# Performance work log

Hardware: AMD Instinct MI355X
Metric: run time of the kernel (lower is better)

Reference implementation:

```python
import jax, jax.numpy as jnp
import numpy as np

H, DK, D, DFF = 8, 64, 512, 512
B, S = 4, 1024
SCALE = 1.0 / np.sqrt(DK)


def _ln(x, g, b, eps=1e-5):
    m = jnp.mean(x, axis=-1, keepdims=True)
    v = jnp.mean((x - m) ** 2, axis=-1, keepdims=True)
    return (x - m) / jnp.sqrt(v + eps) * g + b


def _heads(x, w, b):
    bs, s, _ = x.shape
    return (x @ w + b).reshape(bs, s, H, DK).transpose(0, 2, 1, 3)  # [B,H,S,DK]


def _encoder_layer(x, qw, qb, kw, kb, vw, vb, ow, ob, g1, b1, w1, c1, w2, c2, g2, b2):
    # standard post-LN transformer encoder layer (sub_attention.Encoder(1))
    q = _heads(x, qw, qb)
    k = _heads(x, kw, kb)
    v = _heads(x, vw, vb)
    attn = jax.nn.softmax(jnp.einsum('bhqd,bhkd->bhqk', q, k) * SCALE, axis=-1)
    ctx = jnp.einsum('bhqk,bhkd->bhqd', attn, v).transpose(0, 2, 1, 3).reshape(x.shape[0], -1, H * DK)
    h = _ln(ctx @ ow + ob + x, g1, b1)
    f = jax.nn.relu(h @ w1 + c1) @ w2 + c2
    return _ln(f + h, g2, b2)


def setup_inputs() -> dict:
    key = jax.random.key(0)
    ks = iter(jax.random.split(key, 80))

    def nrm(*shape):
        return jax.random.normal(next(ks), shape, jnp.float32) * 0.02

    inp = {'audio_feat': jax.random.normal(next(ks), (B, S, D), jnp.float32),
           'video_feat': jax.random.normal(next(ks), (B, S, D), jnp.float32)}
    for p in ['aq', 'ak', 'av', 'vq', 'vk', 'vv', 'out']:
        inp[p + '_w'] = nrm(D, D)
        inp[p + '_b'] = jnp.zeros((D,), jnp.float32)
    inp['ln_g'] = jnp.ones((D,), jnp.float32)
    inp['ln_b'] = jnp.zeros((D,), jnp.float32)
    for pfx in ['asa_', 'vsa_']:
        for wn in ['qw', 'kw', 'vw', 'ow']:
            inp[pfx + wn] = nrm(D, D)
        for bn in ['qb', 'kb', 'vb', 'ob']:
            inp[pfx + bn] = jnp.zeros((D,), jnp.float32)
        inp[pfx + 'w1'] = nrm(D, DFF)
        inp[pfx + 'c1'] = jnp.zeros((DFF,), jnp.float32)
        inp[pfx + 'w2'] = nrm(DFF, D)
        inp[pfx + 'c2'] = jnp.zeros((D,), jnp.float32)
        inp[pfx + 'g1'] = jnp.ones((D,), jnp.float32)
        inp[pfx + 'b1'] = jnp.zeros((D,), jnp.float32)
        inp[pfx + 'g2'] = jnp.ones((D,), jnp.float32)
        inp[pfx + 'b2'] = jnp.zeros((D,), jnp.float32)
    return inp


def reference(audio_feat, video_feat, aq_w, aq_b, ak_w, ak_b, av_w, av_b, vq_w, vq_b, vk_w, vk_b, vv_w, vv_b, out_w, out_b, ln_g, ln_b, asa_qw, asa_qb, asa_kw, asa_kb, asa_vw, asa_vb, asa_ow, asa_ob, asa_g1, asa_b1, asa_w1, asa_c1, asa_w2, asa_c2, asa_g2, asa_b2, vsa_qw, vsa_qb, vsa_kw, vsa_kb, vsa_vw, vsa_vb, vsa_ow, vsa_ob, vsa_g1, vsa_b1, vsa_w1, vsa_c1, vsa_w2, vsa_c2, vsa_g2, vsa_b2):
    audio_self = _encoder_layer(audio_feat, asa_qw, asa_qb, asa_kw, asa_kb, asa_vw, asa_vb, asa_ow, asa_ob, asa_g1, asa_b1, asa_w1, asa_c1, asa_w2, asa_c2, asa_g2, asa_b2)
    video_self = _encoder_layer(video_feat, vsa_qw, vsa_qb, vsa_kw, vsa_kb, vsa_vw, vsa_vb, vsa_ow, vsa_ob, vsa_g1, vsa_b1, vsa_w1, vsa_c1, vsa_w2, vsa_c2, vsa_g2, vsa_b2)
    qa = _heads(audio_feat, aq_w, aq_b)
    ka = _heads(audio_feat, ak_w, ak_b)
    va = _heads(audio_feat, av_w, av_b)
    qv = _heads(video_feat, vq_w, vq_b)
    kv = _heads(video_feat, vk_w, vk_b)
    vvh = _heads(video_feat, vv_w, vv_b)
    attn_a = jax.nn.softmax(jnp.einsum('bhqd,bhkd->bhqk', qa, ka) * SCALE, axis=-1)
    attn_v = jax.nn.softmax(jnp.einsum('bhqd,bhkd->bhqk', qv, kv) * SCALE, axis=-1)
    attn = attn_a * attn_v  # dual-softmax elementwise combine
    ctx = jnp.einsum('bhqk,bhkd->bhqd', attn, va) * jnp.einsum('bhqk,bhkd->bhqd', attn, vvh)
    ctx = ctx.transpose(0, 2, 1, 3).reshape(audio_feat.shape[0], -1, H * DK)
    context = ctx @ out_w + out_b
    return _ln(audio_feat + context + audio_self + video_self, ln_g, ln_b)
```

## Files before the change

### kernel.cpp

```cpp
#include <hip/hip_runtime.h>
#include <cstddef>
#include <cstdint>


typedef __attribute__((ext_vector_type(8))) short s8v;
typedef __attribute__((ext_vector_type(4))) float f4v;

#define QSC 0.1803368801111444f
#define EXP2(x) __builtin_amdgcn_exp2f(x)
#define WAITV(N) asm volatile("s_waitcnt vmcnt(" #N ")" ::: "memory")
#define BAR() __builtin_amdgcn_s_barrier()

static __device__ __forceinline__ short f2bf(float f){
  unsigned int u = __builtin_bit_cast(unsigned int, f);
  u += 0x7fffu + ((u >> 16) & 1u);
  return (short)(u >> 16);
}
static __device__ __forceinline__ float bf2f(short s){
  unsigned int u = ((unsigned int)(unsigned short)s) << 16;
  return __builtin_bit_cast(float, u);
}
static __device__ __forceinline__ void gload16(const void* g, void* l){
  __builtin_amdgcn_global_load_lds(
      (const __attribute__((address_space(1))) unsigned int*)g,
      (__attribute__((address_space(3))) unsigned int*)l, 16, 0, 0);
}
#define MFMA16(a,b,c) __builtin_amdgcn_mfma_f32_16x16x32_bf16(a,b,c,0,0,0)

__global__ __launch_bounds__(256) void convert_in(const float* __restrict__ a,
                                                  const float* __restrict__ v,
                                                  short* __restrict__ oa,
                                                  short* __restrict__ ov){
  const float* src = blockIdx.y ? v : a;
  short* dst = blockIdx.y ? ov : oa;
  const int i = (blockIdx.x * 256 + threadIdx.x) * 8;
  float4 x = *reinterpret_cast<const float4*>(src + i);
  float4 y = *reinterpret_cast<const float4*>(src + i + 4);
  s8v o;
  o[0]=f2bf(x.x); o[1]=f2bf(x.y); o[2]=f2bf(x.z); o[3]=f2bf(x.w);
  o[4]=f2bf(y.x); o[5]=f2bf(y.y); o[6]=f2bf(y.z); o[7]=f2bf(y.w);
  *reinterpret_cast<s8v*>(dst + i) = o;
}

struct Ptr19 { const float* p[19]; };
__global__ __launch_bounds__(256) void pack_w(Ptr19 ws, short* __restrict__ wp){
  const int mat = blockIdx.y;
  const float* W = ws.p[mat];
  const int f = blockIdx.x * 256 + threadIdx.x;
  const int nblk = f >> 10, kg = (f >> 4) & 63, nl = f & 15;
  const int n = nblk * 16 + nl, k = kg * 8;
  s8v o;
#pragma unroll
  for (int e = 0; e < 8; ++e) o[e] = f2bf(W[(size_t)(k + e) * 512 + n]);
  *reinterpret_cast<s8v*>(wp + (size_t)mat * 262144 + (size_t)f * 8) = o;
}

struct GemmJobs { const short* A[12]; const short* W[12]; const float* bias[12];
                  short* C[12]; int mode[12]; };

template<bool RELU>
__global__ __launch_bounds__(256) void gemm_bf16(GemmJobs J){
  int i = (blockIdx.z * 32 + blockIdx.y) * 4 + blockIdx.x;
  const int c = (128 * gridDim.z) >> 3;
  i = (i & 7) * c + (i >> 3);
  const int z = i >> 7, rem = i & 127;
  const int by = rem >> 2, bx = rem & 3;

  const short* __restrict__ A = J.A[z];
  const short* __restrict__ Wp = J.W[z];
  const float* __restrict__ bias = J.bias[z];
  short* __restrict__ C = J.C[z];
  const int md = J.mode[z];
  __shared__ short As[2][4096], Bs[2][4096];
  const int tid = threadIdx.x, lane = tid & 63, w = tid >> 6;
  const int wm = w >> 1, wn = w & 1;
  const int m0 = by * 128, n0 = bx * 128;
  const int lh = lane >> 4, ll = lane & 15;
  f4v acc[4][4] = {};

  auto stage = [&](int kt, int buf){
    const int k0 = kt * 32;
#pragma unroll
    for (int p = 0; p < 2; ++p){
      const int f = tid + 256 * p;
      const int blk = f >> 6, kg = (f >> 4) & 3, il = f & 15;
      gload16(A + (size_t)(m0 + blk * 16 + il) * 512 + k0 + kg * 8, &As[buf][f * 8]);
      gload16(Wp + ((size_t)(((n0 >> 4) + blk) * 64 + (k0 >> 3) + kg) * 16 + il) * 8,
              &Bs[buf][f * 8]);
    }
  };

  stage(0, 0);
#pragma unroll
  for (int kt = 0; kt < 16; ++kt){
    if (kt < 15) { stage(kt + 1, (kt + 1) & 1); WAITV(4); }
    else         { WAITV(0); }
    BAR();
    const int cur = kt & 1;
    s8v a[4], b[4];
#pragma unroll
    for (int q = 0; q < 4; ++q)
      a[q] = *reinterpret_cast<const s8v*>(&As[cur][(((wm*4+q)*4 + lh)*16 + ll) * 8]);
#pragma unroll
    for (int j = 0; j < 4; ++j)
      b[j] = *reinterpret_cast<const s8v*>(&Bs[cur][(((wn*4+j)*4 + lh)*16 + ll) * 8]);
#pragma unroll
    for (int q = 0; q < 4; ++q)
#pragma unroll
      for (int j = 0; j < 4; ++j)
        acc[q][j] = MFMA16(a[q], b[j], acc[q][j]);
    BAR();
  }

  if (md == 2){
#pragma unroll
    for (int j = 0; j < 4; ++j){
      const int col = n0 + wn * 64 + j * 16 + ll;
      const float bv = bias[col];
      const int hh = col >> 6, dl = col & 63, dblk = dl >> 4, il = dl & 15;
#pragma unroll
      for (int q = 0; q < 4; ++q){
        const int rowb = m0 + wm * 64 + q * 16 + lh * 4;
#pragma unroll
        for (int r = 0; r < 4; ++r){
          const int m = rowb + r;
          const int bb = m >> 10, srow = m & 1023;
          const size_t off = ((size_t)((bb*8 + hh)*16 + (srow >> 6))) * 4096
                           + (size_t)(((dblk << 7) + (((srow >> 3) & 7) << 4) + il) * 8 + (srow & 7));
          C[off] = f2bf(acc[q][j][r] + bv);
        }
      }
    }
  } else {
    const float sc = (md == 1) ? QSC : 1.0f;
#pragma unroll
    for (int j = 0; j < 4; ++j){
      const int col = n0 + wn * 64 + j * 16 + ll;
      const float bv = bias[col];
#pragma unroll
      for (int q = 0; q < 4; ++q){
        const int rowb = m0 + wm * 64 + q * 16 + lh * 4;
#pragma unroll
        for (int r = 0; r < 4; ++r){
          float v = (acc[q][j][r] + bv) * sc;
          if (RELU) v = fmaxf(v, 0.f);
          C[(size_t)(rowb + r) * 512 + col] = f2bf(v);
        }
      }
    }
  }
}

template<bool RELU>
__global__ __launch_bounds__(256) void gemm_n64(GemmJobs J){
  int i = (blockIdx.z * 32 + blockIdx.y) * 8 + blockIdx.x;
  const int c = (256 * gridDim.z) >> 3;
  i = (i & 7) * c + (i >> 3);
  const int z = i >> 8, rem = i & 255;
  const int by = rem >> 3, bx = rem & 7;

  const short* __restrict__ A = J.A[z];
  const short* __restrict__ Wp = J.W[z];
  const float* __restrict__ bias = J.bias[z];
  short* __restrict__ C = J.C[z];
  __shared__ short As[2][4096], Bs[2][2048];
  const int tid = threadIdx.x, lane = tid & 63, w = tid >> 6;
  const int wm = w >> 1, wn = w & 1;
  const int m0 = by * 128, n0 = bx * 64;
  const int lh = lane >> 4, ll = lane & 15;
  f4v acc[4][2] = {};

  auto stage = [&](int kt, int buf){
    const int k0 = kt * 32;
#pragma unroll
    for (int p = 0; p < 2; ++p){
      const int f = tid + 256 * p;
      const int blk = f >> 6, kg = (f >> 4) & 3, il = f & 15;
      gload16(A + (size_t)(m0 + blk * 16 + il) * 512 + k0 + kg * 8, &As[buf][f * 8]);
    }
    {
      const int f = tid;
      const int blk = f >> 6, kg = (f >> 4) & 3, il = f & 15;
      gload16(Wp + ((size_t)(((n0 >> 4) + blk) * 64 + (k0 >> 3) + kg) * 16 + il) * 8,
              &Bs[buf][f * 8]);
    }
  };

  stage(0, 0);
#pragma unroll
  for (int kt = 0; kt < 16; ++kt){
    if (kt < 15) { stage(kt + 1, (kt + 1) & 1); WAITV(3); }
    else         { WAITV(0); }
    BAR();
    const int cur = kt & 1;
    s8v a[4], b[2];
#pragma unroll
    for (int q = 0; q < 4; ++q)
      a[q] = *reinterpret_cast<const s8v*>(&As[cur][(((wm*4+q)*4 + lh)*16 + ll) * 8]);
#pragma unroll
    for (int j = 0; j < 2; ++j)
      b[j] = *reinterpret_cast<const s8v*>(&Bs[cur][(((wn*2+j)*4 + lh)*16 + ll) * 8]);
#pragma unroll
    for (int q = 0; q < 4; ++q)
#pragma unroll
      for (int j = 0; j < 2; ++j)
        acc[q][j] = MFMA16(a[q], b[j], acc[q][j]);
    BAR();
  }

#pragma unroll
  for (int j = 0; j < 2; ++j){
    const int col = n0 + wn * 32 + j * 16 + ll;
    const float bv = bias[col];
#pragma unroll
    for (int q = 0; q < 4; ++q){
      const int rowb = m0 + wm * 64 + q * 16 + lh * 4;
#pragma unroll
      for (int r = 0; r < 4; ++r){
        float v = acc[q][j][r] + bv;
        if (RELU) v = fmaxf(v, 0.f);
        C[(size_t)(rowb + r) * 512 + col] = f2bf(v);
      }
    }
  }
}

struct AttnJob { const short* Q; const short* K; const short* Vp; short* O; };

__global__ __launch_bounds__(512) void attn_enc(AttnJob j0, AttnJob j1){
  const AttnJob jb = blockIdx.z ? j1 : j0;
  __shared__ short KT[2][4096], VT[2][4096];
  __shared__ short PL[8][1024];
  const int tid = threadIdx.x, lane = tid & 63, w = tid >> 6;
  int bi = blockIdx.y * 8 + blockIdx.x;
  bi = (bi & 7) * 32 + (bi >> 3);
  const int qt = bi & 7, bh = bi >> 3;
  const int b = bh >> 3, h = bh & 7;
  const int q0 = qt * 128;
  const size_t base = (size_t)b * 1024 * 512 + (size_t)h * 64;
  const int lh = lane >> 4, ll = lane & 15;
  short* PLw = PL[w];

  s8v qf[2];
#pragma unroll
  for (int df = 0; df < 2; ++df)
    qf[df] = *reinterpret_cast<const s8v*>(jb.Q + base + (size_t)(q0 + w*16 + ll)*512 + lh*8 + df*32);

  const int sblk = tid >> 7, sg8 = (tid >> 4) & 7, sil = tid & 15;
  auto stage = [&](int it, int buf){
    gload16(jb.K + base + (size_t)(it*64 + sblk*16 + sil)*512 + sg8*8, &KT[buf][tid*8]);
    gload16(jb.Vp + ((size_t)bh*16 + it)*4096 + (size_t)tid*8, &VT[buf][tid*8]);
  };

  f4v o[4] = {};
  float lp[4] = {0.f, 0.f, 0.f, 0.f};

  stage(0, 0);
#pragma unroll 1
  for (int it = 0; it < 16; ++it){
    if (it < 15) { stage(it + 1, (it + 1) & 1); WAITV(2); }
    else         { WAITV(0); }
    BAR();
    const int cur = it & 1;

    f4v s[4] = {};
#pragma unroll
    for (int fn = 0; fn < 4; ++fn)
#pragma unroll
      for (int df = 0; df < 2; ++df){
        s8v kf = *reinterpret_cast<const s8v*>(&KT[cur][((fn*8 + lh + df*4)*16 + ll) * 8]);
        s[fn] = MFMA16(qf[df], kf, s[fn]);
      }

    float px[4][4];
#pragma unroll
    for (int r = 0; r < 4; ++r){
      float p0 = EXP2(s[0][r]), p1 = EXP2(s[1][r]);
      float p2 = EXP2(s[2][r]), p3 = EXP2(s[3][r]);
      px[r][0]=p0; px[r][1]=p1; px[r][2]=p2; px[r][3]=p3;
      lp[r] += (p0 + p1) + (p2 + p3);
    }
#pragma unroll
    for (int r = 0; r < 4; ++r)
#pragma unroll
      for (int fn = 0; fn < 4; ++fn){
        const int q = lh*4 + r, k = fn*16 + ll, kg = k >> 3;
        PLw[(kg*16 + (q ^ kg))*8 + (k & 7)] = f2bf(px[r][fn]);
      }
    s8v pa[2];
#pragma unroll
    for (int kf2 = 0; kf2 < 2; ++kf2){
      const int kg = lh + kf2*4;
      pa[kf2] = *reinterpret_cast<const s8v*>(&PLw[(kg*16 + (ll ^ kg))*8]);
    }
#pragma unroll
    for (int fd = 0; fd < 4; ++fd)
#pragma unroll
      for (int kf2 = 0; kf2 < 2; ++kf2){
        s8v vf = *reinterpret_cast<const s8v*>(&VT[cur][((fd*8 + lh + kf2*4)*16 + ll) * 8]);
        o[fd] = MFMA16(pa[kf2], vf, o[fd]);
      }
    BAR();
  }

#pragma unroll
  for (int r = 0; r < 4; ++r){
    float Z = lp[r];
    Z += __shfl_xor(Z, 1); Z += __shfl_xor(Z, 2);
    Z += __shfl_xor(Z, 4); Z += __shfl_xor(Z, 8);
    const float rz = 1.f / Z;
#pragma unroll
    for (int fd = 0; fd < 4; ++fd)
      jb.O[base + (size_t)(q0 + w*16 + lh*4 + r)*512 + fd*16 + ll] = f2bf(o[fd][r] * rz);
  }
}

__global__ __launch_bounds__(512) void attn_dual(const short* __restrict__ Qa, const short* __restrict__ Ka,
                                                 const short* __restrict__ Vap, const short* __restrict__ Qv,
                                                 const short* __restrict__ Kv, const short* __restrict__ Vvp,
                                                 short* __restrict__ O){
  __shared__ short KTa[2][4096], KTv[2][4096], VTa[2][4096], VTv[2][4096];
  __shared__ short PL[8][1024];
  const int tid = threadIdx.x, lane = tid & 63, w = tid >> 6;
  int bi = blockIdx.y * 8 + blockIdx.x;
  bi = (bi & 7) * 32 + (bi >> 3);
  const int qt = bi & 7, bh = bi >> 3;
  const int b = bh >> 3, h = bh & 7;
  const int q0 = qt * 128;
  const size_t base = (size_t)b * 1024 * 512 + (size_t)h * 64;
  const int lh = lane >> 4, ll = lane & 15;
  short* PLw = PL[w];

  s8v qfa[2], qfv[2];
#pragma unroll
  for (int df = 0; df < 2; ++df){
    const size_t ro = base + (size_t)(q0 + w*16 + ll)*512 + lh*8 + df*32;
    qfa[df] = *reinterpret_cast<const s8v*>(Qa + ro);
    qfv[df] = *reinterpret_cast<const s8v*>(Qv + ro);
  }

  const int sblk = tid >> 7, sg8 = (tid >> 4) & 7, sil = tid & 15;
  auto stage = [&](int it, int buf){
    const size_t krow = base + (size_t)(it*64 + sblk*16 + sil)*512 + sg8*8;
    gload16(Ka + krow, &KTa[buf][tid*8]);
    gload16(Kv + krow, &KTv[buf][tid*8]);
    const size_t voff = ((size_t)bh*16 + it)*4096 + (size_t)tid*8;
    gload16(Vap + voff, &VTa[buf][tid*8]);
    gload16(Vvp + voff, &VTv[buf][tid*8]);
  };

  f4v oa[4] = {}, ov[4] = {};
  float lap[4] = {0,0,0,0}, lvp[4] = {0,0,0,0};

  stage(0, 0);
#pragma unroll 1
  for (int it = 0; it < 16; ++it){
    if (it < 15) { stage(it + 1, (it + 1) & 1); WAITV(4); }
    else         { WAITV(0); }
    BAR();
    const int cur = it & 1;

    f4v sa[4] = {}, sv[4] = {};
#pragma unroll
    for (int fn = 0; fn < 4; ++fn)
#pragma unroll
      for (int df = 0; df < 2; ++df){
        const int boff = ((fn*8 + lh + df*4)*16 + ll) * 8;
        s8v ka = *reinterpret_cast<const s8v*>(&KTa[cur][boff]);
        s8v kv = *reinterpret_cast<const s8v*>(&KTv[cur][boff]);
        sa[fn] = MFMA16(qfa[df], ka, sa[fn]);
        sv[fn] = MFMA16(qfv[df], kv, sv[fn]);
      }

    float pt[4][4];
#pragma unroll
    for (int r = 0; r < 4; ++r){
      float a0 = EXP2(sa[0][r]), a1 = EXP2(sa[1][r]);
      float a2 = EXP2(sa[2][r]), a3 = EXP2(sa[3][r]);
      float v0 = EXP2(sv[0][r]), v1 = EXP2(sv[1][r]);
      float v2 = EXP2(sv[2][r]), v3 = EXP2(sv[3][r]);
      lap[r] += (a0 + a1) + (a2 + a3);
      lvp[r] += (v0 + v1) + (v2 + v3);
      pt[r][0] = a0*v0; pt[r][1] = a1*v1; pt[r][2] = a2*v2; pt[r][3] = a3*v3;
    }
#pragma unroll
    for (int r = 0; r < 4; ++r)
#pragma unroll
      for (int fn = 0; fn < 4; ++fn){
        const int q = lh*4 + r, k = fn*16 + ll, kg = k >> 3;
        PLw[(kg*16 + (q ^ kg))*8 + (k & 7)] = f2bf(pt[r][fn]);
      }
    s8v pa[2];
#pragma unroll
    for (int kf2 = 0; kf2 < 2; ++kf2){
      const int kg = lh + kf2*4;
      pa[kf2] = *reinterpret_cast<const s8v*>(&PLw[(kg*16 + (ll ^ kg))*8]);
    }
#pragma unroll
    for (int fd = 0; fd < 4; ++fd)
#pragma unroll
      for (int kf2 = 0; kf2 < 2; ++kf2){
        const int boff = ((fd*8 + lh + kf2*4)*16 + ll) * 8;
        s8v va = *reinterpret_cast<const s8v*>(&VTa[cur][boff]);
        s8v vv = *reinterpret_cast<const s8v*>(&VTv[cur][boff]);
        oa[fd] = MFMA16(pa[kf2], va, oa[fd]);
        ov[fd] = MFMA16(pa[kf2], vv, ov[fd]);
      }
    BAR();
  }

#pragma unroll
  for (int r = 0; r < 4; ++r){
    float Za = lap[r], Zv = lvp[r];
    Za += __shfl_xor(Za, 1); Za += __shfl_xor(Za, 2);
    Za += __shfl_xor(Za, 4); Za += __shfl_xor(Za, 8);
    Zv += __shfl_xor(Zv, 1); Zv += __shfl_xor(Zv, 2);
    Zv += __shfl_xor(Zv, 4); Zv += __shfl_xor(Zv, 8);
    const float rz = 1.f / (Za * Zv);
#pragma unroll
    for (int fd = 0; fd < 4; ++fd){
      const float v = (oa[fd][r] * rz) * (ov[fd][r] * rz);
      O[base + (size_t)(q0 + w*16 + lh*4 + r)*512 + fd*16 + ll] = f2bf(v);
    }
  }
}

struct LnJob { const short* xb0; const short* xb1; const short* xb2;
               const float* xf; const float* g; const float* bb; void* out; };

template<int NBF, bool ADDF32, bool OUTF32>
__global__ __launch_bounds__(256) void ln_fused(LnJob j0, LnJob j1){
  const LnJob j = blockIdx.y ? j1 : j0;
  const int row = blockIdx.x, t = threadIdx.x;
  const size_t base = (size_t)row * 512;
  float x[2];
#pragma unroll
  for (int u = 0; u < 2; ++u){
    const int c = t + u * 256;
    float v = bf2f(j.xb0[base + c]);
    if (NBF > 1) v += bf2f(j.xb1[base + c]);
    if (NBF > 2) v += bf2f(j.xb2[base + c]);
    if (ADDF32) v += j.xf[base + c];
    x[u] = v;
  }
  float s = x[0] + x[1], ss = x[0]*x[0] + x[1]*x[1];
#pragma unroll
  for (int o = 32; o; o >>= 1){ s += __shfl_xor(s, o); ss += __shfl_xor(ss, o); }
  __shared__ float rb[8];
  const int wv = t >> 6;
  if ((t & 63) == 0){ rb[wv] = s; rb[wv + 4] = ss; }
  __syncthreads();
  s  = rb[0] + rb[1] + rb[2] + rb[3];
  ss = rb[4] + rb[5] + rb[6] + rb[7];
  const float m = s * (1.f / 512.f);
  const float var = ss * (1.f / 512.f) - m * m;
  const float rstd = rsqrtf(var + 1e-5f);
#pragma unroll
  for (int u = 0; u < 2; ++u){
    const int c = t + u * 256;
    const float v = (x[u] - m) * rstd * j.g[c] + j.bb[c];
    if (OUTF32) ((float*)j.out)[base + c] = v;
    else        ((short*)j.out)[base + c] = f2bf(v);
  }
}

extern "C" void kernel_launch(void* const* d_in, const int* in_sizes, int n_in,
                              void* d_out, int out_size, void* d_ws, size_t ws_size,
                              hipStream_t stream) {
  const float* audio = (const float*)d_in[0];
  const float* video = (const float*)d_in[1];
  auto F = [&](int i){ return (const float*)d_in[i]; };

  short* ws16 = (short*)d_ws;
  const size_t SL = 2097152;
  auto S = [&](int i){ return ws16 + (size_t)i * SL; };
  short* Wp = S(12);
  auto WP = [&](int i){ return (const short*)(Wp + (size_t)i * 262144); };
  short* Kcv = (short*)d_out;
  short* Vcv = (short*)d_out + SL;

  convert_in<<<dim3(1024,2), 256, 0, stream>>>(audio, video, S(10), S(11));

  Ptr19 pw;
  const int widx[19] = {18,19,20,21,26,28, 34,35,36,37,42,44, 2,4,6,8,10,12, 14};
  for (int i = 0; i < 19; ++i) pw.p[i] = F(widx[i]);
  pack_w<<<dim3(128,19), 256, 0, stream>>>(pw, Wp);

  GemmJobs g1{};
  const short* g1A[12] = {S(10),S(10),S(10), S(11),S(11),S(11), S(10),S(10),S(10), S(11),S(11),S(11)};
  const short* g1W[12] = {WP(0),WP(1),WP(2), WP(6),WP(7),WP(8), WP(12),WP(13),WP(14), WP(15),WP(16),WP(17)};
  const float* g1B[12] = {F(22),F(23),F(24), F(38),F(39),F(40), F(3),F(5),F(7), F(9),F(11),F(13)};
  short*       g1C[12] = {S(0),S(1),S(2), S(3),S(4),S(5), S(6),S(7),S(8), S(9),Kcv,Vcv};
  const int    g1M[12] = {1,0,2, 1,0,2, 1,0,2, 1,0,2};
  for (int i = 0; i < 12; ++i){ g1.A[i]=g1A[i]; g1.W[i]=g1W[i]; g1.bias[i]=g1B[i]; g1.C[i]=g1C[i]; g1.mode[i]=g1M[i]; }
  gemm_bf16<false><<<dim3(4,32,12), 256, 0, stream>>>(g1);

  attn_enc<<<dim3(8,32,2), 512, 0, stream>>>(AttnJob{S(0),S(1),S(2),S(10)},
                                             AttnJob{S(3),S(4),S(5),S(11)});

  GemmJobs g3{};
  g3.A[0]=S(10); g3.W[0]=WP(3); g3.bias[0]=F(25); g3.C[0]=S(0); g3.mode[0]=0;
  g3.A[1]=S(11); g3.W[1]=WP(9); g3.bias[1]=F(41); g3.C[1]=S(1); g3.mode[1]=0;
  gemm_n64<false><<<dim3(8,32,2), 256, 0, stream>>>(g3);

  ln_fused<1,true,false><<<dim3(4096,2), 256, 0, stream>>>(
      LnJob{S(0),nullptr,nullptr, audio, F(30),F(31), S(2)},
      LnJob{S(1),nullptr,nullptr, video, F(46),F(47), S(3)});

  GemmJobs g5{};
  g5.A[0]=S(2); g5.W[0]=WP(4);  g5.bias[0]=F(27); g5.C[0]=S(4); g5.mode[0]=0;
  g5.A[1]=S(3); g5.W[1]=WP(10); g5.bias[1]=F(43); g5.C[1]=S(5); g5.mode[1]=0;
  gemm_n64<true><<<dim3(8,32,2), 256, 0, stream>>>(g5);

  GemmJobs g6{};
  g6.A[0]=S(4); g6.W[0]=WP(5);  g6.bias[0]=F(29); g6.C[0]=S(0); g6.mode[0]=0;
  g6.A[1]=S(5); g6.W[1]=WP(11); g6.bias[1]=F(45); g6.C[1]=S(1); g6.mode[1]=0;
  gemm_n64<false><<<dim3(8,32,2), 256, 0, stream>>>(g6);

  ln_fused<2,false,false><<<dim3(4096,2), 256, 0, stream>>>(
      LnJob{S(0),S(2),nullptr, nullptr, F(32),F(33), S(4)},
      LnJob{S(1),S(3),nullptr, nullptr, F(48),F(49), S(5)});

  attn_dual<<<dim3(8,32), 512, 0, stream>>>(S(6),S(7),S(8), S(9),Kcv,Vcv, S(3));

  GemmJobs g9{};
  g9.A[0]=S(3); g9.W[0]=WP(18); g9.bias[0]=F(15); g9.C[0]=S(0); g9.mode[0]=0;
  gemm_n64<false><<<dim3(8,32,1), 256, 0, stream>>>(g9);

  LnJob fj{S(0),S(4),S(5), audio, F(16),F(17), d_out};
  ln_fused<3,true,true><<<dim3(4096,1), 256, 0, stream>>>(fj, fj);
}
```

Measured before the change: 200.0 us.

## Stage GEMM epilogues through LDS, merge output GEMMs and fuse final layernorms

The GEMM epilogues now write results into shared memory first and then store them to global memory as 16-byte vectors, replacing scattered 2-byte stores. The head-layout mode writes 4 contiguous shorts per store. The dual-attention kernel moves earlier so its output projection can share one gemm_n64 launch with the two encoder output projections. The second per-encoder layernorm and the final layernorm are folded into one ln_final kernel. Together these cut the launch count and one round trip of intermediate tensors, at the cost of reusing shared buffers and a reshuffled workspace assignment.

```diff
diff --git a/kernel.cpp b/kernel.cpp
--- a/kernel.cpp
+++ b/kernel.cpp
@@ -4,6 +4,7 @@
 
 
 typedef __attribute__((ext_vector_type(8))) short s8v;
+typedef __attribute__((ext_vector_type(4))) short s4v;
 typedef __attribute__((ext_vector_type(4))) float f4v;
 
 #define QSC 0.1803368801111444f
@@ -121,32 +122,35 @@
 #pragma unroll
       for (int q = 0; q < 4; ++q){
         const int rowb = m0 + wm * 64 + q * 16 + lh * 4;
-#pragma unroll
-        for (int r = 0; r < 4; ++r){
-          const int m = rowb + r;
-          const int bb = m >> 10, srow = m & 1023;
-          const size_t off = ((size_t)((bb*8 + hh)*16 + (srow >> 6))) * 4096
-                           + (size_t)(((dblk << 7) + (((srow >> 3) & 7) << 4) + il) * 8 + (srow & 7));
-          C[off] = f2bf(acc[q][j][r] + bv);
-        }
+        const int bb = rowb >> 10, srow = rowb & 1023;
+        const size_t off = ((size_t)((bb*8 + hh)*16 + (srow >> 6))) * 4096
+                         + (size_t)(((dblk << 7) + (((srow >> 3) & 7) << 4) + il) * 8 + (srow & 7));
+        s4v o4;
+#pragma unroll
+        for (int r = 0; r < 4; ++r) o4[r] = f2bf(acc[q][j][r] + bv);
+        *reinterpret_cast<s4v*>(&C[off]) = o4;
       }
     }
   } else {
+    short* epi = (w < 2) ? &As[w][0] : &Bs[w - 2][0];
     const float sc = (md == 1) ? QSC : 1.0f;
 #pragma unroll
     for (int j = 0; j < 4; ++j){
-      const int col = n0 + wn * 64 + j * 16 + ll;
-      const float bv = bias[col];
-#pragma unroll
-      for (int q = 0; q < 4; ++q){
-        const int rowb = m0 + wm * 64 + q * 16 + lh * 4;
+      const float bv = bias[n0 + wn * 64 + j * 16 + ll];
+#pragma unroll
+      for (int q = 0; q < 4; ++q)
 #pragma unroll
         for (int r = 0; r < 4; ++r){
           float v = (acc[q][j][r] + bv) * sc;
           if (RELU) v = fmaxf(v, 0.f);
-          C[(size_t)(rowb + r) * 512 + col] = f2bf(v);
+          epi[(q*16 + lh*4 + r)*64 + j*16 + ll] = f2bf(v);
         }
-      }
+    }
+#pragma unroll
+    for (int i2 = 0; i2 < 8; ++i2){
+      const int row = i2 * 8 + (lane >> 3);
+      s8v vr = *reinterpret_cast<const s8v*>(&epi[row*64 + (lane & 7)*8]);
+      *reinterpret_cast<s8v*>(&C[(size_t)(m0 + wm*64 + row)*512 + n0 + wn*64 + (lane&7)*8]) = vr;
     }
   }
 }
@@ -208,20 +212,24 @@
     BAR();
   }
 
+  short* epi = &As[0][0] + w * 2048;
 #pragma unroll
   for (int j = 0; j < 2; ++j){
-    const int col = n0 + wn * 32 + j * 16 + ll;
-    const float bv = bias[col];
-#pragma unroll
-    for (int q = 0; q < 4; ++q){
-      const int rowb = m0 + wm * 64 + q * 16 + lh * 4;
+    const float bv = bias[n0 + wn * 32 + j * 16 + ll];
+#pragma unroll
+    for (int q = 0; q < 4; ++q)
 #pragma unroll
       for (int r = 0; r < 4; ++r){
         float v = acc[q][j][r] + bv;
         if (RELU) v = fmaxf(v, 0.f);
-        C[(size_t)(rowb + r) * 512 + col] = f2bf(v);
-      }
-    }
+        epi[(q*16 + lh*4 + r)*32 + j*16 + ll] = f2bf(v);
+      }
+  }
+#pragma unroll
+  for (int i2 = 0; i2 < 4; ++i2){
+    const int row = i2 * 16 + (lane >> 2);
+    s8v vr = *reinterpret_cast<const s8v*>(&epi[row*32 + (lane & 3)*8]);
+    *reinterpret_cast<s8v*>(&C[(size_t)(m0 + wm*64 + row)*512 + n0 + wn*32 + (lane&3)*8]) = vr;
   }
 }
 
@@ -464,6 +472,64 @@
   }
 }
 
+__global__ __launch_bounds__(256) void ln_final(const short* __restrict__ fa, const short* __restrict__ ha,
+                                                const short* __restrict__ fv, const short* __restrict__ hv,
+                                                const short* __restrict__ ctx, const float* __restrict__ audio,
+                                                const float* __restrict__ g2a, const float* __restrict__ b2a,
+                                                const float* __restrict__ g2v, const float* __restrict__ b2v,
+                                                const float* __restrict__ gf, const float* __restrict__ bf,
+                                                float* __restrict__ out){
+  const int row = blockIdx.x, t = threadIdx.x;
+  const size_t base = (size_t)row * 512;
+  __shared__ float rb[24];
+  const int wv = t >> 6;
+
+  auto reduce2 = [&](float a, float b, int p){
+    float s = a + b, ss = a*a + b*b;
+#pragma unroll
+    for (int o = 32; o; o >>= 1){ s += __shfl_xor(s, o); ss += __shfl_xor(ss, o); }
+    if ((t & 63) == 0){ rb[p*8 + wv] = s; rb[p*8 + 4 + wv] = ss; }
+  };
+  auto stats = [&](int p, float& m, float& rstd){
+    const float s  = rb[p*8+0] + rb[p*8+1] + rb[p*8+2] + rb[p*8+3];
+    const float ss = rb[p*8+4] + rb[p*8+5] + rb[p*8+6] + rb[p*8+7];
+    m = s * (1.f / 512.f);
+    rstd = rsqrtf(ss * (1.f / 512.f) - m * m + 1e-5f);
+  };
+
+  float xa[2], xv[2];
+#pragma unroll
+  for (int u = 0; u < 2; ++u){
+    const int c = t + u * 256;
+    xa[u] = bf2f(fa[base + c]) + bf2f(ha[base + c]);
+    xv[u] = bf2f(fv[base + c]) + bf2f(hv[base + c]);
+  }
+  reduce2(xa[0], xa[1], 0);
+  reduce2(xv[0], xv[1], 1);
+  __syncthreads();
+  float ma, ra, mv, rv;
+  stats(0, ma, ra);
+  stats(1, mv, rv);
+
+  float xf[2];
+#pragma unroll
+  for (int u = 0; u < 2; ++u){
+    const int c = t + u * 256;
+    const float sa = (xa[u] - ma) * ra * g2a[c] + b2a[c];
+    const float sv = (xv[u] - mv) * rv * g2v[c] + b2v[c];
+    xf[u] = audio[base + c] + bf2f(ctx[base + c]) + sa + sv;
+  }
+  reduce2(xf[0], xf[1], 2);
+  __syncthreads();
+  float mf, rf;
+  stats(2, mf, rf);
+#pragma unroll
+  for (int u = 0; u < 2; ++u){
+    const int c = t + u * 256;
+    out[base + c] = (xf[u] - mf) * rf * gf[c] + bf[c];
+  }
+}
+
 extern "C" void kernel_launch(void* const* d_in, const int* in_sizes, int n_in,
                               void* d_out, int out_size, void* d_ws, size_t ws_size,
                               hipStream_t stream) {
@@ -498,35 +564,29 @@
   attn_enc<<<dim3(8,32,2), 512, 0, stream>>>(AttnJob{S(0),S(1),S(2),S(10)},
                                              AttnJob{S(3),S(4),S(5),S(11)});
 
-  GemmJobs g3{};
-  g3.A[0]=S(10); g3.W[0]=WP(3); g3.bias[0]=F(25); g3.C[0]=S(0); g3.mode[0]=0;
-  g3.A[1]=S(11); g3.W[1]=WP(9); g3.bias[1]=F(41); g3.C[1]=S(1); g3.mode[1]=0;
-  gemm_n64<false><<<dim3(8,32,2), 256, 0, stream>>>(g3);
+  attn_dual<<<dim3(8,32), 512, 0, stream>>>(S(6),S(7),S(8), S(9),Kcv,Vcv, S(0));
+
+  GemmJobs g39{};
+  g39.A[0]=S(10); g39.W[0]=WP(3);  g39.bias[0]=F(25); g39.C[0]=S(1); g39.mode[0]=0;
+  g39.A[1]=S(11); g39.W[1]=WP(9);  g39.bias[1]=F(41); g39.C[1]=S(2); g39.mode[1]=0;
+  g39.A[2]=S(0);  g39.W[2]=WP(18); g39.bias[2]=F(15); g39.C[2]=S(3); g39.mode[2]=0;
+  gemm_n64<false><<<dim3(8,32,3), 256, 0, stream>>>(g39);
 
   ln_fused<1,true,false><<<dim3(4096,2), 256, 0, stream>>>(
-      LnJob{S(0),nullptr,nullptr, audio, F(30),F(31), S(2)},
-      LnJob{S(1),nullptr,nullptr, video, F(46),F(47), S(3)});
+      LnJob{S(1),nullptr,nullptr, audio, F(30),F(31), S(4)},
+      LnJob{S(2),nullptr,nullptr, video, F(46),F(47), S(5)});
 
   GemmJobs g5{};
-  g5.A[0]=S(2); g5.W[0]=WP(4);  g5.bias[0]=F(27); g5.C[0]=S(4); g5.mode[0]=0;
-  g5.A[1]=S(3); g5.W[1]=WP(10); g5.bias[1]=F(43); g5.C[1]=S(5); g5.mode[1]=0;
+  g5.A[0]=S(4); g5.W[0]=WP(4);  g5.bias[0]=F(27); g5.C[0]=S(6); g5.mode[0]=0;
+  g5.A[1]=S(5); g5.W[1]=WP(10); g5.bias[1]=F(43); g5.C[1]=S(7); g5.mode[1]=0;
   gemm_n64<true><<<dim3(8,32,2), 256, 0, stream>>>(g5);
 
   GemmJobs g6{};
-  g6.A[0]=S(4); g6.W[0]=WP(5);  g6.bias[0]=F(29); g6.C[0]=S(0); g6.mode[0]=0;
-  g6.A[1]=S(5); g6.W[1]=WP(11); g6.bias[1]=F(45); g6.C[1]=S(1); g6.mode[1]=0;
+  g6.A[0]=S(6); g6.W[0]=WP(5);  g6.bias[0]=F(29); g6.C[0]=S(8); g6.mode[0]=0;
+  g6.A[1]=S(7); g6.W[1]=WP(11); g6.bias[1]=F(45); g6.C[1]=S(9); g6.mode[1]=0;
   gemm_n64<false><<<dim3(8,32,2), 256, 0, stream>>>(g6);
 
-  ln_fused<2,false,false><<<dim3(4096,2), 256, 0, stream>>>(
-      LnJob{S(0),S(2),nullptr, nullptr, F(32),F(33), S(4)},
-      LnJob{S(1),S(3),nullptr, nullptr, F(48),F(49), S(5)});
-
-  attn_dual<<<dim3(8,32), 512, 0, stream>>>(S(6),S(7),S(8), S(9),Kcv,Vcv, S(3));
-
-  GemmJobs g9{};
-  g9.A[0]=S(3); g9.W[0]=WP(18); g9.bias[0]=F(15); g9.C[0]=S(0); g9.mode[0]=0;
-  gemm_n64<false><<<dim3(8,32,1), 256, 0, stream>>>(g9);
-
-  LnJob fj{S(0),S(4),S(5), audio, F(16),F(17), d_out};
-  ln_fused<3,true,true><<<dim3(4096,1), 256, 0, stream>>>(fj, fj);
-}
+  ln_final<<<4096, 256, 0, stream>>>(S(8),S(4), S(9),S(5), S(3), audio,
+                                     F(32),F(33), F(48),F(49), F(16),F(17),
+                                     (float*)d_out);
+}
```

New measurement: 183.0 us. 8.5% less time.
